# Kernel optimization log

Measured on AMD Instinct MI355X. Metric: run time of the kernel, lower is better.

The kernel has to match this reference:

```python
import jax, jax.numpy as jnp
import numpy as np

B, L = 2, 2048
DIM, VOCAB, NL = 1024, 32000, 4
DSTATE, DCONV, EXPAND, HEADDIM = 128, 4, 2, 64
DIN = EXPAND * DIM            # 2048
H = DIN // HEADDIM            # 32 heads
CONVDIM = DIN + 2 * DSTATE    # 2304
DPROJ = 2 * DIN + 2 * DSTATE + H  # 4384
FFN = 4 * DIM                 # 4096
Q = 128                       # SSD chunk size
EPS = 1e-6


def _rms(x):
    return x * jax.lax.rsqrt(jnp.mean(x * x, axis=-1, keepdims=True) + EPS)


def _causal_conv(x, w, b):
    # x [B,L,C], depthwise causal conv, w [C,DCONV], b [C]
    y = jax.lax.conv_general_dilated(
        x.transpose(0, 2, 1), w[:, None, :], (1,), [(DCONV - 1, 0)],
        dimension_numbers=('NCH', 'OIH', 'NCH'), feature_group_count=CONVDIM)
    return (y + b[:, None]).transpose(0, 2, 1)


def _ssd(x, dt, A, Bm, Cm):
    # Exact selective scan h_t = h_{t-1}*exp(dt_t*A) + dt_t * x_t B_t ; y_t = C_t . h_t
    # computed in chunked (SSD) matmul form. x [b,l,h,p], dt [b,l,h], A [h], Bm/Cm [b,l,n]
    b, l, h, p = x.shape
    n = Bm.shape[-1]
    c = l // Q
    xr = x.reshape(b, c, Q, h, p)
    dtr = dt.reshape(b, c, Q, h)
    ar = (dt * A).reshape(b, c, Q, h)          # per-step log-decay (<= 0)
    Br = Bm.reshape(b, c, Q, n)
    Cr = Cm.reshape(b, c, Q, n)
    ca = jnp.cumsum(ar, axis=2)                # inclusive cumulative log-decay
    # ---- intra-chunk: causal decay-weighted 'attention' ----
    cah = ca.transpose(0, 1, 3, 2)             # [b,c,h,Q]
    idx = jnp.arange(Q)
    mask = idx[:, None] >= idx[None, :]
    diff = jnp.where(mask[None, None, None], cah[..., :, None] - cah[..., None, :], -jnp.inf)
    M = jnp.exp(diff)                          # [b,c,h,Q,Q]
    CB = jnp.einsum('bcin,bcjn->bcij', Cr, Br)
    T = CB[:, :, None] * M                     # [b,c,h,Q,Q]
    y_intra = jnp.einsum('bchij,bcjh,bcjhp->bcihp', T, dtr, xr)
    # ---- chunk-final states ----
    w = jnp.exp(ca[:, :, -1:, :] - ca) * dtr   # [b,c,Q,h]
    states = jnp.einsum('bcjh,bcjn,bcjhp->bchpn', w, Br, xr)
    chunk_decay = jnp.exp(ca[:, :, -1, :])     # [b,c,h]
    def step(s, inp):
        cd, st = inp
        prev = s
        s = s * cd[:, :, None, None] + st
        return s, prev
    s0 = jnp.zeros((b, h, p, n), x.dtype)
    _, s_prev = jax.lax.scan(step, s0, (chunk_decay.transpose(1, 0, 2),
                                        states.transpose(1, 0, 2, 3, 4)))
    s_prev = s_prev.transpose(1, 0, 2, 3, 4)   # [b,c,h,p,n] state entering each chunk
    y_inter = jnp.einsum('bcih,bcin,bchpn->bcihp', jnp.exp(ca), Cr, s_prev)
    return (y_intra + y_inter).reshape(b, l, h, p)


def _mamba(x, Wi, cw, cb, dtb, Alog, Dp, nw, Wo):
    bsz, sl, _ = x.shape
    zxbcdt = x @ Wi.T                          # [b,l,DPROJ]
    z = zxbcdt[..., :DIN]
    xBC = zxbcdt[..., DIN:DIN + CONVDIM]
    dtraw = zxbcdt[..., DIN + CONVDIM:]
    xBC = jax.nn.silu(_causal_conv(xBC, cw, cb))
    xs = xBC[..., :DIN]
    Bm = xBC[..., DIN:DIN + DSTATE]
    Cm = xBC[..., DIN + DSTATE:]
    dt = jax.nn.softplus(dtraw + dtb)
    A = -jnp.exp(Alog)
    x4 = xs.reshape(bsz, sl, H, HEADDIM)
    y = _ssd(x4, dt, A, Bm, Cm) + Dp[None, None, :, None] * x4
    y = y.reshape(bsz, sl, DIN)
    yg = y * jax.nn.silu(z)                    # gated RMSNorm (norm_before_gate=False)
    y = _rms(yg) * nw
    return y @ Wo.T


def _forward(tokens, embedding, lm_head_bias, in_proj_w, conv_w, conv_b,
             dt_bias, A_log, D, mnorm_w, out_proj_w, u_w, v_w, o_w):
    x = embedding[tokens]
    for li in range(NL):
        for _ in range(2):  # original applies each (mamba, ffn) pair twice
            x = _rms(x)
            x = x + _mamba(x, in_proj_w[li], conv_w[li], conv_b[li], dt_bias[li],
                           A_log[li], D[li], mnorm_w[li], out_proj_w[li])
            x = _rms(x)
            x = x + ((x @ u_w[li].T) * (x @ v_w[li].T)) @ o_w[li].T  # SGLU, dropout=0
    return x @ embedding.T + lm_head_bias      # tied lm_head


def setup_inputs():
    key = jax.random.key(0)
    ks = jax.random.split(key, 16)
    s = 0.02
    return {
        'tokens': jax.random.randint(ks[0], (B, L), 0, VOCAB),
        'embedding': jax.random.normal(ks[1], (VOCAB, DIM), jnp.float32) * s,
        'lm_head_bias': jnp.zeros((VOCAB,), jnp.float32),
        'in_proj_w': jax.random.normal(ks[2], (NL, DPROJ, DIM), jnp.float32) * s,
        'conv_w': jax.random.normal(ks[3], (NL, CONVDIM, DCONV), jnp.float32) * 0.2,
        'conv_b': jnp.zeros((NL, CONVDIM), jnp.float32),
        'dt_bias': jax.random.normal(ks[4], (NL, H), jnp.float32) * 0.3 - 3.0,
        'A_log': jnp.log(jax.random.uniform(ks[5], (NL, H), jnp.float32, 1.0, 16.0)),
        'D': jnp.ones((NL, H), jnp.float32) + 0.1 * jax.random.normal(ks[6], (NL, H), jnp.float32),
        'mnorm_w': jnp.ones((NL, DIN), jnp.float32),
        'out_proj_w': jax.random.normal(ks[7], (NL, DIM, DIN), jnp.float32) * s,
        'u_w': jax.random.normal(ks[8], (NL, FFN, DIM), jnp.float32) * s,
        'v_w': jax.random.normal(ks[9], (NL, FFN, DIM), jnp.float32) * s,
        'o_w': jax.random.normal(ks[10], (NL, DIM, FFN), jnp.float32) * s,
    }


def reference(tokens, embedding, lm_head_bias, in_proj_w, conv_w, conv_b,
              dt_bias, A_log, D, mnorm_w, out_proj_w, u_w, v_w, o_w):
    return _forward(tokens, embedding, lm_head_bias, in_proj_w, conv_w, conv_b,
                    dt_bias, A_log, D, mnorm_w, out_proj_w, u_w, v_w, o_w)
```

## Files before the change

### kernel.cpp

```cpp
#include <hip/hip_runtime.h>
#include <hip/hip_bf16.h>

#define BSZ 2
#define LSEQ 2048
#define DIM 1024
#define VOCAB 32000
#define NLAYER 4
#define DSTATE 128
#define DCONV 4
#define HEADDIM 64
#define DIN 2048
#define NH 32
#define CONVDIM 2304
#define DPROJ 4384
#define FFN 4096
#define QLEN 128
#define NTOK 4096
#define NCHUNK 32
#define CPB 16

#define SMEM_BYTES 147456
#define SMEM2 131072

using f32x4 = __attribute__((ext_vector_type(4))) float;
using f16   = _Float16;
using f16x4 = __attribute__((ext_vector_type(4))) _Float16;
using f16x8 = __attribute__((ext_vector_type(8))) _Float16;

__device__ __forceinline__ void gld16(const void* g, void* l) {
  __builtin_amdgcn_global_load_lds(
      (const __attribute__((address_space(1))) unsigned int*)g,
      (__attribute__((address_space(3))) unsigned int*)l, 16, 0, 0);
}

__device__ __forceinline__ void swz_tiles(int& bx, int& by) {
  const int nx = gridDim.x, ny = gridDim.y;
  const int nwg = nx * ny;
  int bid = blockIdx.y * nx + blockIdx.x;
  if ((nwg & 7) == 0) bid = (bid & 7) * (nwg >> 3) + (bid >> 3);
  const int CW = 8;
  const int nchx = nx / CW;
  const int per = CW * ny;
  const int ch = bid / per;
  if (ch < nchx) {
    int wi = bid - ch * per;
    bx = ch * CW + (wi & (CW - 1));
    by = wi / CW;
  } else {
    int tb = bid - nchx * per;
    int tw = nx - nchx * CW;
    bx = nchx * CW + (tb % tw);
    by = tb / tw;
  }
}

template <int MODE>
__global__ __launch_bounds__(512, 2) void gemm_p(
    const f16* __restrict__ A, const f16* __restrict__ Bu, const f16* __restrict__ Bv,
    float* __restrict__ Cf, f16* __restrict__ Gh, const float* __restrict__ bias,
    int N, int Ksub, int lda, int ldb, int ldc)
{
  extern __shared__ char smem[];
  const int tid  = threadIdx.x;
  const int lane = tid & 63;
  const int wid  = tid >> 6;
  int bx, by; swz_tiles(bx, by);
  const int m0 = by * 256;
  const int n0 = bx * 128;
  const size_t kbase = (size_t)blockIdx.z * Ksub;
  if (gridDim.z > 1) Cf += (size_t)blockIdx.z * (size_t)gridDim.y * 256 * ldc;

  const int NT  = Ksub >> 6;
  const int NTT = (MODE == 2) ? 2 * NT : NT;

  int arA[4], acA[4];
#pragma unroll
  for (int L = 0; L < 4; ++L) {
    int q = L * 512 + tid;
    int row = q >> 3;
    arA[L] = m0 + row;
    acA[L] = ((q & 7) ^ (row & 7)) << 3;
  }
  int brB[2], bcB[2];
#pragma unroll
  for (int L = 0; L < 2; ++L) {
    int q = L * 512 + tid;
    int row = q >> 3;
    int r = n0 + row; if (r > N - 1) r = N - 1;
    brB[L] = r;
    bcB[L] = ((q & 7) ^ (row & 7)) << 3;
  }

  auto stage = [&](int tt) {
    const int b = tt - (tt / 3) * 3;
    char* Ad = smem + b * 32768;
    char* Bd = smem + 98304 + b * 16384;
    int ta = tt;
    const f16* Bp = Bu;
    if (MODE == 2 && tt >= NT) { ta = tt - NT; Bp = Bv; }
    const int kb = ta << 6;
#pragma unroll
    for (int L = 0; L < 4; ++L)
      gld16(A + (size_t)arA[L] * lda + kbase + kb + acA[L], Ad + (L * 512 + tid) * 16);
#pragma unroll
    for (int L = 0; L < 2; ++L)
      gld16(Bp + (size_t)brB[L] * ldb + kbase + kb + bcB[L], Bd + (L * 512 + tid) * 16);
  };

  const int wm = (wid >> 1) << 6;
  const int wn = (wid & 1) << 6;
  const int fr = lane & 15;
  const int kg = lane >> 4;

  f32x4 accu[4][4] = {};
  f32x4 accv[4][4] = {};

  stage(0);
  stage(1);

  for (int t = 0; t < NTT; ++t) {
    const int b = t - (t / 3) * 3;
    if (t + 2 < NTT) {
      stage(t + 2);
      asm volatile("s_waitcnt vmcnt(12)" ::: "memory");
    } else if (t + 1 < NTT) {
      asm volatile("s_waitcnt vmcnt(6)" ::: "memory");
    } else {
      asm volatile("s_waitcnt vmcnt(0)" ::: "memory");
    }
    __builtin_amdgcn_s_barrier();
    asm volatile("" ::: "memory");
    const f16* Ab = (const f16*)(smem + b * 32768);
    const f16* Bb = (const f16*)(smem + 98304 + b * 16384);
#pragma unroll
    for (int s = 0; s < 2; ++s) {
      f16x8 af[4], bf[4];
#pragma unroll
      for (int j = 0; j < 4; ++j) {
        int row = wm + j * 16 + fr;
        int g = kg + s * 4;
        af[j] = *(const f16x8*)&Ab[row * 64 + ((g ^ (row & 7)) << 3)];
      }
#pragma unroll
      for (int i = 0; i < 4; ++i) {
        int row = wn + i * 16 + fr;
        int g = kg + s * 4;
        bf[i] = *(const f16x8*)&Bb[row * 64 + ((g ^ (row & 7)) << 3)];
      }
      if (MODE == 2 && t >= NT) {
#pragma unroll
        for (int i = 0; i < 4; ++i)
#pragma unroll
          for (int j = 0; j < 4; ++j)
            accv[i][j] = __builtin_amdgcn_mfma_f32_16x16x32_f16(bf[i], af[j], accv[i][j], 0, 0, 0);
      } else {
#pragma unroll
        for (int i = 0; i < 4; ++i)
#pragma unroll
          for (int j = 0; j < 4; ++j)
            accu[i][j] = __builtin_amdgcn_mfma_f32_16x16x32_f16(bf[i], af[j], accu[i][j], 0, 0, 0);
      }
    }
    asm volatile("" ::: "memory");
    __builtin_amdgcn_s_barrier();
    asm volatile("" ::: "memory");
  }

  const int c4 = kg << 2;
  if constexpr (MODE == 0) {
#pragma unroll
    for (int i = 0; i < 4; ++i) {
      const int col = n0 + wn + i * 16 + c4;
      if (col >= N) continue;
      f32x4 bv = bias ? *(const f32x4*)(bias + col) : f32x4{0, 0, 0, 0};
#pragma unroll
      for (int j = 0; j < 4; ++j) {
        const int row = m0 + wm + j * 16 + fr;
        *(f32x4*)(Cf + (size_t)row * ldc + col) = accu[i][j] + bv;
      }
    }
  } else {
#pragma unroll
    for (int i = 0; i < 4; ++i) {
      const int col = n0 + wn + i * 16 + c4;
#pragma unroll
      for (int j = 0; j < 4; ++j) {
        const int row = m0 + wm + j * 16 + fr;
        f16x4 h;
#pragma unroll
        for (int r = 0; r < 4; ++r)
          h[r] = (f16)(accu[i][j][r] * accv[i][j][r]);
        *(f16x4*)(Gh + (size_t)row * ldc + col) = h;
      }
    }
  }
}

__global__ __launch_bounds__(512, 2) void gemm_p2(
    const f16* __restrict__ A, const f16* __restrict__ B,
    float* __restrict__ Cf, const float* __restrict__ bias,
    int N, int Ksub, int lda, int ldb, int ldc)
{
  extern __shared__ char smem[];
  const int tid  = threadIdx.x;
  const int lane = tid & 63;
  const int wid  = tid >> 6;
  int bx, by; swz_tiles(bx, by);
  const int m0 = by * 256;
  const int n0 = bx * 256;
  const size_t kbase = (size_t)blockIdx.z * Ksub;
  if (gridDim.z > 1) Cf += (size_t)blockIdx.z * (size_t)gridDim.y * 256 * ldc;
  const int NT = Ksub >> 6;

  int arA[4], acA[4], brB[4], bcB[4];
#pragma unroll
  for (int L = 0; L < 4; ++L) {
    int q = L * 512 + tid;
    int row = q >> 3;
    arA[L] = m0 + row;
    acA[L] = ((q & 7) ^ (row & 7)) << 3;
    int r = n0 + row; if (r > N - 1) r = N - 1;
    brB[L] = r;
    bcB[L] = acA[L];
  }

  auto stage = [&](int tt) {
    const int b = tt & 1;
    char* Ad = smem + b * 65536;
    char* Bd = Ad + 32768;
    const int kb = tt << 6;
#pragma unroll
    for (int L = 0; L < 4; ++L)
      gld16(A + (size_t)arA[L] * lda + kbase + kb + acA[L], Ad + (L * 512 + tid) * 16);
#pragma unroll
    for (int L = 0; L < 4; ++L)
      gld16(B + (size_t)brB[L] * ldb + kbase + kb + bcB[L], Bd + (L * 512 + tid) * 16);
  };

  const int wm = (wid >> 2) << 7;
  const int wn = (wid & 3) << 6;
  const int fr = lane & 15;
  const int kg = lane >> 4;

  f32x4 acc[4][8] = {};

  stage(0);

  for (int t = 0; t < NT; ++t) {
    if (t + 1 < NT) {
      stage(t + 1);
      asm volatile("s_waitcnt vmcnt(8)" ::: "memory");
    } else {
      asm volatile("s_waitcnt vmcnt(0)" ::: "memory");
    }
    __builtin_amdgcn_s_barrier();
    asm volatile("" ::: "memory");
    const f16* Ab = (const f16*)(smem + (t & 1) * 65536);
    const f16* Bb = Ab + 16384;
#pragma unroll
    for (int s = 0; s < 2; ++s) {
      const int g = kg + s * 4;
      f16x8 af[8], bf[4];
#pragma unroll
      for (int j = 0; j < 8; ++j) {
        int row = wm + j * 16 + fr;
        af[j] = *(const f16x8*)&Ab[row * 64 + ((g ^ (row & 7)) << 3)];
      }
#pragma unroll
      for (int i = 0; i < 4; ++i) {
        int row = wn + i * 16 + fr;
        bf[i] = *(const f16x8*)&Bb[row * 64 + ((g ^ (row & 7)) << 3)];
      }
#pragma unroll
      for (int i = 0; i < 4; ++i)
#pragma unroll
        for (int j = 0; j < 8; ++j)
          acc[i][j] = __builtin_amdgcn_mfma_f32_16x16x32_f16(bf[i], af[j], acc[i][j], 0, 0, 0);
    }
    asm volatile("" ::: "memory");
    __builtin_amdgcn_s_barrier();
    asm volatile("" ::: "memory");
  }

  const int c4 = kg << 2;
#pragma unroll
  for (int i = 0; i < 4; ++i) {
    const int col = n0 + wn + i * 16 + c4;
    if (col >= N) continue;
    f32x4 bv = bias ? *(const f32x4*)(bias + col) : f32x4{0, 0, 0, 0};
#pragma unroll
    for (int j = 0; j < 8; ++j) {
      const int row = m0 + wm + j * 16 + fr;
      *(f32x4*)(Cf + (size_t)row * ldc + col) = acc[i][j] + bv;
    }
  }
}

template <bool DORMS>
__global__ __launch_bounds__(256) void reduce_rms(const float* __restrict__ parts,
                                                  const float* __restrict__ resid,
                                                  float* __restrict__ xn,
                                                  f16* __restrict__ outh, int np)
{
  const int row = blockIdx.x, tid = threadIdx.x;
  const size_t base = (size_t)row * DIM + tid * 4;
  f32x4 s = *(const f32x4*)(resid + base);
  for (int p = 0; p < np; ++p)
    s += *(const f32x4*)(parts + (size_t)p * (NTOK * DIM) + base);
  if constexpr (!DORMS) {
    f16x4 h;
#pragma unroll
    for (int c = 0; c < 4; ++c) h[c] = (f16)s[c];
    *(f16x4*)(outh + base) = h;
    return;
  }
  float ss = s[0] * s[0] + s[1] * s[1] + s[2] * s[2] + s[3] * s[3];
  for (int o = 32; o; o >>= 1) ss += __shfl_down(ss, o);
  __shared__ float red[4];
  if ((tid & 63) == 0) red[tid >> 6] = ss;
  __syncthreads();
  ss = red[0] + red[1] + red[2] + red[3];
  const float sc = rsqrtf(ss * (1.f / 1024.f) + 1e-6f);
  f32x4 o4 = s * sc;
  *(f32x4*)(xn + base) = o4;
  f16x4 h;
#pragma unroll
  for (int c = 0; c < 4; ++c) h[c] = (f16)o4[c];
  *(f16x4*)(outh + base) = h;
}

__global__ __launch_bounds__(256) void cvt_f2h_k(const float* __restrict__ src,
                                                 f16* __restrict__ dst, int n)
{
  for (size_t i = ((size_t)blockIdx.x * 256 + threadIdx.x) * 4; i < (size_t)n;
       i += (size_t)gridDim.x * 1024) {
    f32x4 v = *(const f32x4*)(src + i);
    f16x4 o;
#pragma unroll
    for (int c = 0; c < 4; ++c) o[c] = (f16)v[c];
    *(f16x4*)(dst + i) = o;
  }
}

__global__ __launch_bounds__(256) void cvt_wts(
    const float* __restrict__ inw, const float* __restrict__ outw,
    const float* __restrict__ uw, const float* __restrict__ vw,
    const float* __restrict__ ow,
    f16* __restrict__ w_in, f16* __restrict__ w_out,
    f16* __restrict__ w_uv, f16* __restrict__ w_o)
{
  const int b = blockIdx.x;
  const float* src; f16* dst; int base;
  if (b < 4384)       { src = inw;  dst = w_in;                       base = 0; }
  else if (b < 6432)  { src = outw; dst = w_out;                      base = 4384; }
  else if (b < 10528) { src = uw;   dst = w_uv;                       base = 6432; }
  else if (b < 14624) { src = vw;   dst = w_uv + (size_t)FFN * DIM;   base = 10528; }
  else                { src = ow;   dst = w_o;                        base = 14624; }
  const size_t i = ((size_t)(b - base) * 256 + threadIdx.x) * 4;
  f32x4 v = *(const f32x4*)(src + i);
  f16x4 o;
#pragma unroll
  for (int c = 0; c < 4; ++c) o[c] = (f16)v[c];
  *(f16x4*)(dst + i) = o;
}

__global__ __launch_bounds__(256) void gather_k(const int* __restrict__ tok,
                                                const float* __restrict__ emb,
                                                float* __restrict__ x)
{
  const int row = blockIdx.x;
  const int t = tok[row];
  const f32x4* s = (const f32x4*)(emb + (size_t)t * DIM);
  f32x4* d = (f32x4*)(x + (size_t)row * DIM);
  d[threadIdx.x] = s[threadIdx.x];
}

__global__ __launch_bounds__(256) void rms1024(const float* __restrict__ in,
                                               float* __restrict__ outf,
                                               f16* __restrict__ outh)
{
  const int row = blockIdx.x, tid = threadIdx.x;
  f32x4 v = ((const f32x4*)(in + (size_t)row * DIM))[tid];
  float ss = v[0] * v[0] + v[1] * v[1] + v[2] * v[2] + v[3] * v[3];
  for (int o = 32; o; o >>= 1) ss += __shfl_down(ss, o);
  __shared__ float red[4];
  if ((tid & 63) == 0) red[tid >> 6] = ss;
  __syncthreads();
  ss = red[0] + red[1] + red[2] + red[3];
  const float sc = rsqrtf(ss * (1.f / 1024.f) + 1e-6f);
  f32x4 o4 = v * sc;
  ((f32x4*)(outf + (size_t)row * DIM))[tid] = o4;
  f16x4 h;
#pragma unroll
  for (int c = 0; c < 4; ++c) h[c] = (f16)o4[c];
  ((f16x4*)(outh + (size_t)row * DIM))[tid] = h;
}

__global__ __launch_bounds__(256) void convdt(const float* __restrict__ zx,
                                              const float* __restrict__ cw,
                                              const float* __restrict__ cbias,
                                              const float* __restrict__ dtb,
                                              const float* __restrict__ alog,
                                              float* __restrict__ xbc,
                                              float* __restrict__ dt,
                                              float* __restrict__ ca)
{
  if (blockIdx.x < 576) {
    const int sid = blockIdx.x * 256 + threadIdx.x;
    const int c0 = (sid % 576) * 4;
    const int t0 = (sid / 576) * 16;
    float w[4][4], bs[4];
#pragma unroll
    for (int cc = 0; cc < 4; ++cc) {
      f32x4 wv = *(const f32x4*)(cw + (size_t)(c0 + cc) * 4);
      w[cc][0] = wv[0]; w[cc][1] = wv[1]; w[cc][2] = wv[2]; w[cc][3] = wv[3];
      bs[cc] = cbias[c0 + cc];
    }
    const int l0 = t0 & (LSEQ - 1);
    f32x4 x3 = {0, 0, 0, 0}, x2 = {0, 0, 0, 0}, x1 = {0, 0, 0, 0};
    if (l0 != 0) {
      x3 = *(const f32x4*)(zx + (size_t)(t0 - 3) * DPROJ + DIN + c0);
      x2 = *(const f32x4*)(zx + (size_t)(t0 - 2) * DPROJ + DIN + c0);
      x1 = *(const f32x4*)(zx + (size_t)(t0 - 1) * DPROJ + DIN + c0);
    }
    for (int i = 0; i < 16; ++i) {
      const int t = t0 + i;
      f32x4 xc = *(const f32x4*)(zx + (size_t)t * DPROJ + DIN + c0);
      f32x4 o;
#pragma unroll
      for (int cc = 0; cc < 4; ++cc) {
        float a = bs[cc] + x3[cc] * w[cc][0] + x2[cc] * w[cc][1] +
                  x1[cc] * w[cc][2] + xc[cc] * w[cc][3];
        o[cc] = a / (1.f + expf(-a));
      }
      *(f32x4*)(xbc + (size_t)t * CONVDIM + c0) = o;
      x3 = x2; x2 = x1; x1 = xc;
    }
  } else {
    const int loc = (threadIdx.x >> 7) * 128;
    const int u = (blockIdx.x - 576) * 2 + (threadIdx.x >> 7);
    const int bc = u >> 5, h = u & 31, q = threadIdx.x & 127;
    const int t = bc * 128 + q;
    float raw = zx[(size_t)t * DPROJ + (DIN + CONVDIM) + h] + dtb[h];
    float d = raw > 20.f ? raw : log1pf(expf(raw));
    dt[t * 32 + h] = d;
    float a = -expf(alog[h]) * d;
    __shared__ float s[256];
    s[loc + q] = a;
    __syncthreads();
    for (int off = 1; off < 128; off <<= 1) {
      float v = (q >= off) ? s[loc + q - off] : 0.f;
      __syncthreads();
      s[loc + q] += v;
      __syncthreads();
    }
    ca[(size_t)u * 128 + q] = s[loc + q];
  }
}

__global__ __launch_bounds__(256) void cb_mfma(const float* __restrict__ xbc,
                                               float* __restrict__ CBo)
{
  const int bc = blockIdx.x;
  __shared__ f16 Cm[128 * 72], Bm[128 * 72];
  const int tid = threadIdx.x, lane = tid & 63, wid = tid >> 6;
  const int fr = lane & 15, kg = lane >> 4;
  f32x4 acc[2][8] = {};
  const int i = tid & 127;
  const float* rowp = xbc + (size_t)(bc * 128 + i) * CONVDIM + DIN;

  for (int kh = 0; kh < 2; ++kh) {
#pragma unroll
    for (int it = 0; it < 8; ++it) {
      int idx = it * 256 + tid;
      int n0 = (idx >> 7) * 4;
      f32x4 bv = *(const f32x4*)(rowp + kh * 64 + n0);
      f32x4 cv = *(const f32x4*)(rowp + DSTATE + kh * 64 + n0);
      f16x4 hb, hc;
#pragma unroll
      for (int c = 0; c < 4; ++c) { hb[c] = (f16)bv[c]; hc[c] = (f16)cv[c]; }
      *(f16x4*)&Bm[i * 72 + n0] = hb;
      *(f16x4*)&Cm[i * 72 + n0] = hc;
    }
    __syncthreads();
#pragma unroll
    for (int kf = 0; kf < 2; ++kf) {
      const int ko = kf * 32 + kg * 8;
      f16x8 cf[2], bf[8];
#pragma unroll
      for (int ii = 0; ii < 2; ++ii)
        cf[ii] = *(const f16x8*)&Cm[((wid * 2 + ii) * 16 + fr) * 72 + ko];
#pragma unroll
      for (int jj = 0; jj < 8; ++jj)
        bf[jj] = *(const f16x8*)&Bm[(jj * 16 + fr) * 72 + ko];
#pragma unroll
      for (int ii = 0; ii < 2; ++ii)
#pragma unroll
        for (int jj = 0; jj < 8; ++jj)
          acc[ii][jj] = __builtin_amdgcn_mfma_f32_16x16x32_f16(cf[ii], bf[jj], acc[ii][jj], 0, 0, 0);
    }
    __syncthreads();
  }
  float* out = CBo + (size_t)bc * 16384;
#pragma unroll
  for (int ii = 0; ii < 2; ++ii) {
    const int i0 = (wid * 2 + ii) * 16 + kg * 4;
#pragma unroll
    for (int jj = 0; jj < 8; ++jj) {
      const int j = jj * 16 + fr;
#pragma unroll
      for (int r = 0; r < 4; ++r)
        out[(size_t)(i0 + r) * 128 + j] = acc[ii][jj][r];
    }
  }
}

__global__ __launch_bounds__(256) void ssd_states(const float* __restrict__ xbc,
                                                  const float* __restrict__ dt,
                                                  const float* __restrict__ ca,
                                                  float* __restrict__ ST)
{
  const int bc = blockIdx.x >> 5, h = blockIdx.x & 31;
  __shared__ f16 Am[128 * 136];
  __shared__ f16 Bm[64 * 136];
  __shared__ float warr[128];
  const int tid = threadIdx.x, lane = tid & 63, wid = tid >> 6;
  if (tid < 128) {
    float cv = ca[(size_t)blockIdx.x * 128 + tid];
    float cl = ca[(size_t)blockIdx.x * 128 + 127];
    warr[tid] = expf(cl - cv) * dt[(size_t)(bc * 128 + tid) * 32 + h];
  }
  __syncthreads();
  {
    const int j = tid & 127;
    const float wj = warr[j];
    const float* br = xbc + (size_t)(bc * 128 + j) * CONVDIM + DIN;
#pragma unroll
    for (int it = 0; it < 16; ++it) {
      int idx = it * 256 + tid;
      int n0 = (idx >> 7) * 4;
      f32x4 v = *(const f32x4*)(br + n0);
#pragma unroll
      for (int c = 0; c < 4; ++c) Am[(n0 + c) * 136 + j] = (f16)(v[c] * wj);
    }
    const float* xr = xbc + (size_t)(bc * 128 + j) * CONVDIM + h * 64;
#pragma unroll
    for (int it = 0; it < 8; ++it) {
      int idx = it * 256 + tid;
      int p0 = (idx >> 7) * 4;
      f32x4 v = *(const f32x4*)(xr + p0);
#pragma unroll
      for (int c = 0; c < 4; ++c) Bm[(p0 + c) * 136 + j] = (f16)v[c];
    }
  }
  __syncthreads();
  const int fr = lane & 15, kg = lane >> 4;
  f32x4 acc[2][4] = {};
#pragma unroll
  for (int kf = 0; kf < 4; ++kf) {
    const int ko = kf * 32 + kg * 8;
    f16x8 bw[2], xf[4];
#pragma unroll
    for (int ii = 0; ii < 2; ++ii)
      bw[ii] = *(const f16x8*)&Am[((wid * 2 + ii) * 16 + fr) * 136 + ko];
#pragma unroll
    for (int pi = 0; pi < 4; ++pi)
      xf[pi] = *(const f16x8*)&Bm[(pi * 16 + fr) * 136 + ko];
#pragma unroll
    for (int ii = 0; ii < 2; ++ii)
#pragma unroll
      for (int pi = 0; pi < 4; ++pi)
        acc[ii][pi] = __builtin_amdgcn_mfma_f32_16x16x32_f16(bw[ii], xf[pi], acc[ii][pi], 0, 0, 0);
  }
  float* sb = ST + (size_t)blockIdx.x * 8192;
#pragma unroll
  for (int ii = 0; ii < 2; ++ii) {
    const int n0 = (wid * 2 + ii) * 16 + kg * 4;
#pragma unroll
    for (int pi = 0; pi < 4; ++pi) {
      const int p = pi * 16 + fr;
      *(f32x4*)(sb + (size_t)p * 128 + n0) = acc[ii][pi];
    }
  }
}

__global__ __launch_bounds__(256) void scan_k(const float* __restrict__ ca,
                                              float* __restrict__ states)
{
  const int b = blockIdx.x >> 10, h = (blockIdx.x >> 5) & 31, seg = blockIdx.x & 31;
  const int e = seg * 256 + threadIdx.x;
  float s = 0.f;
  for (int c = 0; c < CPB; ++c) {
    int bc = b * CPB + c;
    float cd = expf(ca[(size_t)(bc * 32 + h) * 128 + 127]);
    size_t idx = (size_t)(bc * 32 + h) * 8192 + e;
    float v = states[idx];
    states[idx] = s;
    s = s * cd + v;
  }
}

__global__ __launch_bounds__(256) void ssd_y(const float* __restrict__ xbc,
                                             const float* __restrict__ dt,
                                             const float* __restrict__ ca,
                                             const float* __restrict__ CB,
                                             const float* __restrict__ Dvec,
                                             const float* __restrict__ ST,
                                             float* __restrict__ ybuf)
{
  const int bc = blockIdx.x >> 5, h = blockIdx.x & 31;
  __shared__ f16 Am[128 * 136];
  __shared__ f16 Bm[64 * 136];
  __shared__ float cas[128], dtl[128];
  const int tid = threadIdx.x, lane = tid & 63, wid = tid >> 6;
  if (tid < 128) {
    cas[tid] = ca[(size_t)blockIdx.x * 128 + tid];
    dtl[tid] = dt[(size_t)(bc * 128 + tid) * 32 + h];
  }
  __syncthreads();
  {
    const int j = tid & 127;
    const float dj = dtl[j];
    const float* xr = xbc + (size_t)(bc * 128 + j) * CONVDIM + h * 64;
#pragma unroll
    for (int it = 0; it < 8; ++it) {
      int idx = it * 256 + tid;
      int p0 = (idx >> 7) * 4;
      f32x4 v = *(const f32x4*)(xr + p0);
#pragma unroll
      for (int c = 0; c < 4; ++c) Bm[(p0 + c) * 136 + j] = (f16)(v[c] * dj);
    }
  }
  {
    const int i = tid >> 1;
    const int jh = (tid & 1) * 64;
    const float cai = cas[i];
    const float* cbr = CB + (size_t)bc * 16384 + (size_t)i * 128 + jh;
#pragma unroll
    for (int g = 0; g < 8; ++g) {
      int j0 = g * 8;
      f32x4 v0 = *(const f32x4*)(cbr + j0);
      f32x4 v1 = *(const f32x4*)(cbr + j0 + 4);
      f16x8 tv;
#pragma unroll
      for (int c = 0; c < 8; ++c) {
        int j = jh + j0 + c;
        float cbv = (c < 4) ? v0[c] : v1[c - 4];
        float val = (j <= i) ? cbv * expf(cai - cas[j]) : 0.f;
        tv[c] = (f16)val;
      }
      *(f16x8*)&Am[i * 136 + jh + j0] = tv;
    }
  }
  __syncthreads();
  const int fr = lane & 15, kg = lane >> 4;
  f32x4 a1[2][4] = {}, a2[2][4] = {};
#pragma unroll
  for (int kf = 0; kf < 4; ++kf) {
    const int ko = kf * 32 + kg * 8;
    f16x8 xf[4], tf[2];
#pragma unroll
    for (int pi = 0; pi < 4; ++pi)
      xf[pi] = *(const f16x8*)&Bm[(pi * 16 + fr) * 136 + ko];
#pragma unroll
    for (int ii = 0; ii < 2; ++ii)
      tf[ii] = *(const f16x8*)&Am[((wid * 2 + ii) * 16 + fr) * 136 + ko];
#pragma unroll
    for (int ii = 0; ii < 2; ++ii)
#pragma unroll
      for (int pi = 0; pi < 4; ++pi)
        a1[ii][pi] = __builtin_amdgcn_mfma_f32_16x16x32_f16(xf[pi], tf[ii], a1[ii][pi], 0, 0, 0);
  }
  __syncthreads();
  {
    const int i = tid & 127;
    const float* cr = xbc + (size_t)(bc * 128 + i) * CONVDIM + DIN + DSTATE;
#pragma unroll
    for (int it = 0; it < 16; ++it) {
      int idx = it * 256 + tid;
      int n0 = (idx >> 7) * 4;
      f32x4 v = *(const f32x4*)(cr + n0);
      f16x4 hv;
#pragma unroll
      for (int c = 0; c < 4; ++c) hv[c] = (f16)v[c];
      *(f16x4*)&Am[i * 136 + n0] = hv;
    }
    const float* sr = ST + (size_t)blockIdx.x * 8192;
    const int p = tid & 63;
#pragma unroll
    for (int it = 0; it < 8; ++it) {
      int idx = it * 256 + tid;
      int n0 = (idx >> 6) * 4;
      f32x4 v = *(const f32x4*)(sr + (size_t)p * 128 + n0);
      f16x4 hv;
#pragma unroll
      for (int c = 0; c < 4; ++c) hv[c] = (f16)v[c];
      *(f16x4*)&Bm[p * 136 + n0] = hv;
    }
  }
  __syncthreads();
#pragma unroll
  for (int kf = 0; kf < 4; ++kf) {
    const int ko = kf * 32 + kg * 8;
    f16x8 sf[4], cf[2];
#pragma unroll
    for (int pi = 0; pi < 4; ++pi)
      sf[pi] = *(const f16x8*)&Bm[(pi * 16 + fr) * 136 + ko];
#pragma unroll
    for (int ii = 0; ii < 2; ++ii)
      cf[ii] = *(const f16x8*)&Am[((wid * 2 + ii) * 16 + fr) * 136 + ko];
#pragma unroll
    for (int ii = 0; ii < 2; ++ii)
#pragma unroll
      for (int pi = 0; pi < 4; ++pi)
        a2[ii][pi] = __builtin_amdgcn_mfma_f32_16x16x32_f16(sf[pi], cf[ii], a2[ii][pi], 0, 0, 0);
  }
  const float dh = Dvec[h];
#pragma unroll
  for (int ii = 0; ii < 2; ++ii) {
    const int i = (wid * 2 + ii) * 16 + fr;
    const float ei = expf(cas[i]);
    const int tg = bc * 128 + i;
#pragma unroll
    for (int pi = 0; pi < 4; ++pi) {
      const int p0 = pi * 16 + kg * 4;
      f32x4 xv = *(const f32x4*)(xbc + (size_t)tg * CONVDIM + h * 64 + p0);
      f32x4 y = a1[ii][pi] + ei * a2[ii][pi] + dh * xv;
      *(f32x4*)(ybuf + (size_t)tg * DIN + h * 64 + p0) = y;
    }
  }
}

__global__ __launch_bounds__(256) void gate_rms(const float* __restrict__ ybuf,
                                                const float* __restrict__ zx,
                                                const float* __restrict__ nw,
                                                f16* __restrict__ outh)
{
  const int row = blockIdx.x, tid = threadIdx.x;
  const float* yr = ybuf + (size_t)row * DIN;
  const float* zr = zx + (size_t)row * DPROJ;
  f32x4 y0 = *(const f32x4*)(yr + tid * 4);
  f32x4 y1 = *(const f32x4*)(yr + 1024 + tid * 4);
  f32x4 z0 = *(const f32x4*)(zr + tid * 4);
  f32x4 z1 = *(const f32x4*)(zr + 1024 + tid * 4);
  f32x4 g0, g1;
#pragma unroll
  for (int c = 0; c < 4; ++c) {
    g0[c] = y0[c] * (z0[c] / (1.f + expf(-z0[c])));
    g1[c] = y1[c] * (z1[c] / (1.f + expf(-z1[c])));
  }
  float ss = 0.f;
#pragma unroll
  for (int c = 0; c < 4; ++c) ss += g0[c] * g0[c] + g1[c] * g1[c];
  for (int o = 32; o; o >>= 1) ss += __shfl_down(ss, o);
  __shared__ float red[4];
  if ((tid & 63) == 0) red[tid >> 6] = ss;
  __syncthreads();
  ss = red[0] + red[1] + red[2] + red[3];
  const float sc = rsqrtf(ss * (1.f / 2048.f) + 1e-6f);
  f32x4 w0 = *(const f32x4*)(nw + tid * 4);
  f32x4 w1 = *(const f32x4*)(nw + 1024 + tid * 4);
  f16x4 h0, h1;
#pragma unroll
  for (int c = 0; c < 4; ++c) {
    h0[c] = (f16)(g0[c] * sc * w0[c]);
    h1[c] = (f16)(g1[c] * sc * w1[c]);
  }
  *(f16x4*)(outh + (size_t)row * DIN + tid * 4) = h0;
  *(f16x4*)(outh + (size_t)row * DIN + 1024 + tid * 4) = h1;
}

extern "C" void kernel_launch(void* const* d_in, const int* in_sizes, int n_in,
                              void* d_out, int out_size, void* d_ws, size_t ws_size,
                              hipStream_t stream)
{
  (void)in_sizes; (void)n_in; (void)out_size; (void)ws_size;
  const int*   tokens = (const int*)d_in[0];
  const float* emb    = (const float*)d_in[1];
  const float* lmb    = (const float*)d_in[2];
  const float* inw    = (const float*)d_in[3];
  const float* cw     = (const float*)d_in[4];
  const float* cbias  = (const float*)d_in[5];
  const float* dtb    = (const float*)d_in[6];
  const float* alog   = (const float*)d_in[7];
  const float* Dvec   = (const float*)d_in[8];
  const float* nw     = (const float*)d_in[9];
  const float* outw   = (const float*)d_in[10];
  const float* uw     = (const float*)d_in[11];
  const float* vw     = (const float*)d_in[12];
  const float* ow     = (const float*)d_in[13];

  char* ws = (char*)d_ws;
  size_t off = 0;
  auto alloc = [&](size_t bytes) { void* p = ws + off; off += (bytes + 255) & ~(size_t)255; return p; };
  f16* emb_h  = (f16*)alloc((size_t)VOCAB * DIM * 2);
  f16* w_in   = (f16*)alloc((size_t)DPROJ * DIM * 2);
  f16* w_out  = (f16*)alloc((size_t)DIM * DIN * 2);
  f16* w_uv   = (f16*)alloc((size_t)2 * FFN * DIM * 2);
  f16* w_o    = (f16*)alloc((size_t)DIM * FFN * 2);
  float* xbuf = (float*)alloc((size_t)NTOK * DIM * 4);
  float* xn   = (float*)alloc((size_t)NTOK * DIM * 4);
  f16* xnh    = (f16*)alloc((size_t)NTOK * DIM * 2);
  f16* xh_lm  = (f16*)alloc((size_t)NTOK * DIM * 2);
  float* dtbuf = (float*)alloc((size_t)NTOK * NH * 4);
  float* cabuf = (float*)alloc((size_t)NCHUNK * NH * QLEN * 4);
  float* CBbuf = (float*)alloc((size_t)NCHUNK * QLEN * QLEN * 4);
  f16* abh    = (f16*)alloc((size_t)NTOK * FFN * 2);

  char* ob = (char*)d_out;
  float* states = (float*)(ob);
  float* zxb    = (float*)(ob + 134217728);
  float* xbc    = (float*)(ob + 206045184);
  float* ybuf   = (float*)(ob + 243793920);
  float* parts  = (float*)(ob + 277348352);

  cvt_f2h_k<<<4096, 256, 0, stream>>>(emb, emb_h, VOCAB * DIM);
  gather_k<<<NTOK, 256, 0, stream>>>(tokens, emb, xbuf);
  rms1024<<<NTOK, 256, 0, stream>>>(xbuf, xn, xnh);

  for (int it = 0; it < 2 * NLAYER; ++it) {
    const int li = it >> 1;
    if ((it & 1) == 0) {
      cvt_wts<<<18720, 256, 0, stream>>>(
          inw + (size_t)li * DPROJ * DIM, outw + (size_t)li * DIM * DIN,
          uw + (size_t)li * FFN * DIM, vw + (size_t)li * FFN * DIM,
          ow + (size_t)li * DIM * FFN, w_in, w_out, w_uv, w_o);
    }
    gemm_p<0><<<dim3((DPROJ + 127) / 128, NTOK / 256, 1), 512, SMEM_BYTES, stream>>>(
        xnh, w_in, nullptr, zxb, nullptr, nullptr, DPROJ, DIM, DIM, DIM, DPROJ);
    convdt<<<1088, 256, 0, stream>>>(zxb, cw + (size_t)li * CONVDIM * DCONV,
                                     cbias + (size_t)li * CONVDIM,
                                     dtb + li * NH, alog + li * NH, xbc, dtbuf, cabuf);
    cb_mfma<<<NCHUNK, 256, 0, stream>>>(xbc, CBbuf);
    ssd_states<<<NCHUNK * NH, 256, 0, stream>>>(xbc, dtbuf, cabuf, states);
    scan_k<<<2048, 256, 0, stream>>>(cabuf, states);
    ssd_y<<<NCHUNK * NH, 256, 0, stream>>>(xbc, dtbuf, cabuf, CBbuf,
                                           Dvec + li * NH, states, ybuf);
    gate_rms<<<NTOK, 256, 0, stream>>>(ybuf, zxb, nw + (size_t)li * DIN, abh);
    gemm_p<0><<<dim3(DIM / 128, NTOK / 256, 2), 512, SMEM_BYTES, stream>>>(
        abh, w_out, nullptr, parts, nullptr, nullptr, DIM, DIN / 2, DIN, DIN, DIM);
    reduce_rms<true><<<NTOK, 256, 0, stream>>>(parts, xn, xn, xnh, 2);
    gemm_p<2><<<dim3(FFN / 128, NTOK / 256, 1), 512, SMEM_BYTES, stream>>>(
        xnh, w_uv, w_uv + (size_t)FFN * DIM, nullptr, abh, nullptr, FFN, DIM, DIM, DIM, FFN);
    gemm_p<0><<<dim3(DIM / 128, NTOK / 256, 2), 512, SMEM_BYTES, stream>>>(
        abh, w_o, nullptr, parts, nullptr, nullptr, DIM, FFN / 2, FFN, FFN, DIM);
    if (it < 2 * NLAYER - 1)
      reduce_rms<true><<<NTOK, 256, 0, stream>>>(parts, xn, xn, xnh, 2);
    else
      reduce_rms<false><<<NTOK, 256, 0, stream>>>(parts, xn, nullptr, xh_lm, 2);
  }

  gemm_p2<<<dim3(VOCAB / 256, NTOK / 256, 1), 512, SMEM2, stream>>>(
      xh_lm, emb_h, (float*)d_out, lmb, VOCAB, DIM, DIM, DIM, VOCAB);
}
```

Baseline: 3.362 ms.

## Add dedicated dual-B u/v gated GEMM and raise wave priority around MFMA blocks

Replaces the generic MODE 2 gated GEMM for the FFN u/v projection with a new kernel that loads both the u and v weight tiles for each K step together. It accumulates both products in the same loop over K and writes the fp16 product directly. This drops the doubled K loop that alternated between u and v and reuses each A fragment for both products. Separately, s_setprio is raised around MFMA bursts in all matmul kernels to favour issuing math over memory instructions. The new kernel doubles accumulator register use, which may hurt occupancy.

```diff
diff --git a/kernel.cpp b/kernel.cpp
--- a/kernel.cpp
+++ b/kernel.cpp
@@ -147,6 +147,7 @@
         int g = kg + s * 4;
         bf[i] = *(const f16x8*)&Bb[row * 64 + ((g ^ (row & 7)) << 3)];
       }
+      __builtin_amdgcn_s_setprio(1);
       if (MODE == 2 && t >= NT) {
 #pragma unroll
         for (int i = 0; i < 4; ++i)
@@ -160,6 +161,7 @@
           for (int j = 0; j < 4; ++j)
             accu[i][j] = __builtin_amdgcn_mfma_f32_16x16x32_f16(bf[i], af[j], accu[i][j], 0, 0, 0);
       }
+      __builtin_amdgcn_s_setprio(0);
     }
     asm volatile("" ::: "memory");
     __builtin_amdgcn_s_barrier();
@@ -271,11 +273,13 @@
         int row = wn + i * 16 + fr;
         bf[i] = *(const f16x8*)&Bb[row * 64 + ((g ^ (row & 7)) << 3)];
       }
+      __builtin_amdgcn_s_setprio(1);
 #pragma unroll
       for (int i = 0; i < 4; ++i)
 #pragma unroll
         for (int j = 0; j < 8; ++j)
           acc[i][j] = __builtin_amdgcn_mfma_f32_16x16x32_f16(bf[i], af[j], acc[i][j], 0, 0, 0);
+      __builtin_amdgcn_s_setprio(0);
     }
     asm volatile("" ::: "memory");
     __builtin_amdgcn_s_barrier();
@@ -292,6 +296,113 @@
     for (int j = 0; j < 8; ++j) {
       const int row = m0 + wm + j * 16 + fr;
       *(f32x4*)(Cf + (size_t)row * ldc + col) = acc[i][j] + bv;
+    }
+  }
+}
+
+__global__ __launch_bounds__(512, 2) void gemm_uv2(
+    const f16* __restrict__ A, const f16* __restrict__ Bu, const f16* __restrict__ Bv,
+    f16* __restrict__ Gh)
+{
+  extern __shared__ char smem[];
+  const int tid  = threadIdx.x;
+  const int lane = tid & 63;
+  const int wid  = tid >> 6;
+  int bx, by; swz_tiles(bx, by);
+  const int m0 = by * 256;
+  const int n0 = bx * 128;
+  const int NT = DIM >> 6;
+
+  int arA[4], acA[4];
+  const f16* bp[4];
+  int bcB[4];
+#pragma unroll
+  for (int L = 0; L < 4; ++L) {
+    int q = L * 512 + tid;
+    int row = q >> 3;
+    arA[L] = m0 + row;
+    acA[L] = ((q & 7) ^ (row & 7)) << 3;
+    bcB[L] = acA[L];
+    bp[L] = (row < 128) ? (Bu + (size_t)(n0 + row) * DIM)
+                        : (Bv + (size_t)(n0 + row - 128) * DIM);
+  }
+
+  auto stage = [&](int tt) {
+    const int b = tt & 1;
+    char* Ad = smem + b * 65536;
+    char* Bd = Ad + 32768;
+    const int kb = tt << 6;
+#pragma unroll
+    for (int L = 0; L < 4; ++L)
+      gld16(A + (size_t)arA[L] * DIM + kb + acA[L], Ad + (L * 512 + tid) * 16);
+#pragma unroll
+    for (int L = 0; L < 4; ++L)
+      gld16(bp[L] + kb + bcB[L], Bd + (L * 512 + tid) * 16);
+  };
+
+  const int wm = (wid >> 1) << 6;
+  const int wn = (wid & 1) << 6;
+  const int fr = lane & 15;
+  const int kg = lane >> 4;
+
+  f32x4 accu[4][4] = {}, accv[4][4] = {};
+
+  stage(0);
+
+  for (int t = 0; t < NT; ++t) {
+    if (t + 1 < NT) {
+      stage(t + 1);
+      asm volatile("s_waitcnt vmcnt(8)" ::: "memory");
+    } else {
+      asm volatile("s_waitcnt vmcnt(0)" ::: "memory");
+    }
+    __builtin_amdgcn_s_barrier();
+    asm volatile("" ::: "memory");
+    const f16* Ab = (const f16*)(smem + (t & 1) * 65536);
+    const f16* Bb = Ab + 16384;
+#pragma unroll
+    for (int s = 0; s < 2; ++s) {
+      const int g = kg + s * 4;
+      f16x8 af[4], bfu[4], bfv[4];
+#pragma unroll
+      for (int j = 0; j < 4; ++j) {
+        int row = wm + j * 16 + fr;
+        af[j] = *(const f16x8*)&Ab[row * 64 + ((g ^ (row & 7)) << 3)];
+      }
+#pragma unroll
+      for (int i = 0; i < 4; ++i) {
+        int ru = wn + i * 16 + fr;
+        int rv = 128 + wn + i * 16 + fr;
+        bfu[i] = *(const f16x8*)&Bb[ru * 64 + ((g ^ (ru & 7)) << 3)];
+        bfv[i] = *(const f16x8*)&Bb[rv * 64 + ((g ^ (rv & 7)) << 3)];
+      }
+      __builtin_amdgcn_s_setprio(1);
+#pragma unroll
+      for (int i = 0; i < 4; ++i)
+#pragma unroll
+        for (int j = 0; j < 4; ++j) {
+          accu[i][j] = __builtin_amdgcn_mfma_f32_16x16x32_f16(bfu[i], af[j], accu[i][j], 0, 0, 0);
+          accv[i][j] = __builtin_amdgcn_mfma_f32_16x16x32_f16(bfv[i], af[j], accv[i][j], 0, 0, 0);
+        }
+      __builtin_amdgcn_s_setprio(0);
+    }
+    asm volatile("" ::: "memory");
+    __builtin_amdgcn_s_barrier();
+    asm volatile("" ::: "memory");
+  }
+
+  const int c4 = kg << 2;
+#pragma unroll
+  for (int i = 0; i < 4; ++i) {
+    const int col = n0 + wn + i * 16 + c4;
+#pragma unroll
+    for (int j = 0; j < 4; ++j) {
+      const int row = m0 + wm + j * 16 + fr;
+      f16x4 h;
+#pragma unroll
+      for (int r = 0; r < 4; ++r)
+        h[r] = (f16)(accu[i][j][r] * accv[i][j][r]);
+      *(f16x4*)(Gh + (size_t)row * FFN + col) = h;
     }
   }
 }
@@ -493,11 +604,13 @@
 #pragma unroll
       for (int jj = 0; jj < 8; ++jj)
         bf[jj] = *(const f16x8*)&Bm[(jj * 16 + fr) * 72 + ko];
+      __builtin_amdgcn_s_setprio(1);
 #pragma unroll
       for (int ii = 0; ii < 2; ++ii)
 #pragma unroll
         for (int jj = 0; jj < 8; ++jj)
           acc[ii][jj] = __builtin_amdgcn_mfma_f32_16x16x32_f16(cf[ii], bf[jj], acc[ii][jj], 0, 0, 0);
+      __builtin_amdgcn_s_setprio(0);
     }
     __syncthreads();
   }
@@ -566,11 +679,13 @@
 #pragma unroll
     for (int pi = 0; pi < 4; ++pi)
       xf[pi] = *(const f16x8*)&Bm[(pi * 16 + fr) * 136 + ko];
+    __builtin_amdgcn_s_setprio(1);
 #pragma unroll
     for (int ii = 0; ii < 2; ++ii)
 #pragma unroll
       for (int pi = 0; pi < 4; ++pi)
         acc[ii][pi] = __builtin_amdgcn_mfma_f32_16x16x32_f16(bw[ii], xf[pi], acc[ii][pi], 0, 0, 0);
+    __builtin_amdgcn_s_setprio(0);
   }
   float* sb = ST + (size_t)blockIdx.x * 8192;
 #pragma unroll
@@ -665,11 +780,13 @@
 #pragma unroll
     for (int ii = 0; ii < 2; ++ii)
       tf[ii] = *(const f16x8*)&Am[((wid * 2 + ii) * 16 + fr) * 136 + ko];
+    __builtin_amdgcn_s_setprio(1);
 #pragma unroll
     for (int ii = 0; ii < 2; ++ii)
 #pragma unroll
       for (int pi = 0; pi < 4; ++pi)
         a1[ii][pi] = __builtin_amdgcn_mfma_f32_16x16x32_f16(xf[pi], tf[ii], a1[ii][pi], 0, 0, 0);
+    __builtin_amdgcn_s_setprio(0);
   }
   __syncthreads();
   {
@@ -709,11 +826,13 @@
 #pragma unroll
     for (int ii = 0; ii < 2; ++ii)
       cf[ii] = *(const f16x8*)&Am[((wid * 2 + ii) * 16 + fr) * 136 + ko];
+    __builtin_amdgcn_s_setprio(1);
 #pragma unroll
     for (int ii = 0; ii < 2; ++ii)
 #pragma unroll
       for (int pi = 0; pi < 4; ++pi)
         a2[ii][pi] = __builtin_amdgcn_mfma_f32_16x16x32_f16(sf[pi], cf[ii], a2[ii][pi], 0, 0, 0);
+    __builtin_amdgcn_s_setprio(0);
   }
   const float dh = Dvec[h];
 #pragma unroll
@@ -840,8 +959,8 @@
     gemm_p<0><<<dim3(DIM / 128, NTOK / 256, 2), 512, SMEM_BYTES, stream>>>(
         abh, w_out, nullptr, parts, nullptr, nullptr, DIM, DIN / 2, DIN, DIN, DIM);
     reduce_rms<true><<<NTOK, 256, 0, stream>>>(parts, xn, xn, xnh, 2);
-    gemm_p<2><<<dim3(FFN / 128, NTOK / 256, 1), 512, SMEM_BYTES, stream>>>(
-        xnh, w_uv, w_uv + (size_t)FFN * DIM, nullptr, abh, nullptr, FFN, DIM, DIM, DIM, FFN);
+    gemm_uv2<<<dim3(FFN / 128, NTOK / 256, 1), 512, SMEM2, stream>>>(
+        xnh, w_uv, w_uv + (size_t)FFN * DIM, abh);
     gemm_p<0><<<dim3(DIM / 128, NTOK / 256, 2), 512, SMEM_BYTES, stream>>>(
         abh, w_o, nullptr, parts, nullptr, nullptr, DIM, FFN / 2, FFN, FFN, DIM);
     if (it < 2 * NLAYER - 1)
```

New measurement: 3.289 ms. 1.02x faster.
